# Optimization experiments

Hardware: AMD Instinct MI355X
Metric: run time of the kernel (lower is better)

## Reference

```python
import jax, jax.numpy as jnp
import numpy as np

B, DV, W, H = 256, 2048, 14, 14
DA = 620            # answer embedding dim
DATT = 1200         # attention dim_v == dim_a == dim_mm (elementwise fusion)
DOUT = 1024         # vec2seq dim_v / dim_a
NUM_CLASSES = 3000


def setup_inputs() -> dict:
    key = jax.random.key(0)
    ks = jax.random.split(key, 14)
    s = lambda *sh: 1.0 / np.sqrt(sh[-1])
    return {
        "input_v": jax.random.normal(ks[0], (B, DV, W, H), jnp.float32),
        "emb": jax.random.normal(ks[1], (NUM_CLASSES, DA), jnp.float32),
        "W_conv_v": jax.random.normal(ks[2], (DATT, DV), jnp.float32) * s(DV),
        "b_conv_v": jnp.zeros((DATT,), jnp.float32),
        "W_lin_a": jax.random.normal(ks[3], (DATT, DA), jnp.float32) * s(DA),
        "b_lin_a": jnp.zeros((DATT,), jnp.float32),
        "w_att": jax.random.normal(ks[4], (DATT,), jnp.float32) * s(DATT),
        "b_att": jnp.zeros((), jnp.float32),
        "W_img": jax.random.normal(ks[5], (DOUT, DV), jnp.float32) * s(DV),
        "b_img": jnp.zeros((DOUT,), jnp.float32),
        "W_ans": jax.random.normal(ks[6], (DOUT, DA), jnp.float32) * s(DA),
        "b_ans": jnp.zeros((DOUT,), jnp.float32),
        "input_a": jax.random.randint(ks[7], (B,), 0, NUM_CLASSES, jnp.int64)
                   if jax.config.jax_enable_x64 else
                   jax.random.randint(ks[7], (B,), 0, NUM_CLASSES, jnp.int32),
    }


def reference(input_v, emb, W_conv_v, b_conv_v, W_lin_a, b_lin_a,
              w_att, b_att, W_img, b_img, W_ans, b_ans, input_a):
    # answer embedding lookup: [B, DA]
    x_a_vec = emb[input_a]

    # --- _attention ---
    # original visual features flattened: [B, WH, DV]
    x_v_orig = input_v.reshape(B, DV, W * H).transpose(0, 2, 1)
    # conv1x1 + relu on image map -> [B, WH, DATT]
    x_v = jax.nn.relu(jnp.einsum('bchw,kc->bhwk', input_v, W_conv_v) + b_conv_v)
    x_v = x_v.reshape(B, W * H, DATT)
    # linear + relu on answer vec -> [B, DATT]
    x_a = jax.nn.relu(x_a_vec @ W_lin_a.T + b_lin_a)
    # elementwise fusion (MLB-style) + relu -> [B, WH, DATT]
    x_att = jax.nn.relu(x_v * x_a[:, None, :])
    # conv_att (1x1 conv, 1 output channel) -> logits [B, WH]
    logits = jnp.einsum('bsk,k->bs', x_att, w_att) + b_att
    attn = jax.nn.softmax(logits, axis=-1)             # [B, WH]
    # attention-weighted sum over spatial positions -> [B, DV]
    x_v_att = jnp.einsum('bs,bsd->bd', attn, x_v_orig)

    # --- prepare_feature ---
    v_feat = x_v_att @ W_img.T + b_img                 # [B, DOUT]
    a_feat = x_a_vec @ W_ans.T + b_ans                 # [B, DOUT]
    return jnp.concatenate([v_feat, a_feat], axis=-1)  # [B, 2*DOUT]
```

## Files before the change

kernel.cpp:

```cpp
#include <hip/hip_runtime.h>
#include <cstdint>
#include <cstddef>

#define B_     256
#define S_     196
#define DV_    2048
#define DA_    620
#define DATT_  1200
#define DATTP_ 1280
#define DOUT_  1024

#define IVB_SSTR 224

typedef unsigned short ushort_t;
typedef __attribute__((ext_vector_type(8))) short short8;
typedef __attribute__((ext_vector_type(4))) float floatx4;

__device__ __forceinline__ float bf2f(unsigned int u) {
    union { unsigned int i; float f; } v; v.i = u << 16; return v.f;
}
__device__ __forceinline__ ushort_t f2bf(float x) {
    union { float f; unsigned int u; } c; c.f = x;
    unsigned int r = (c.u + 0x7fffu + ((c.u >> 16) & 1u)) >> 16;
    return (ushort_t)r;
}

struct F4 { float v[4]; };
struct F8 { float v[8]; };

__device__ __forceinline__ F4 ld4(const void* p, size_t i, int f) {
    F4 r;
    if (f) {
        float4 u = *(const float4*)((const float*)p + i);
        r.v[0]=u.x; r.v[1]=u.y; r.v[2]=u.z; r.v[3]=u.w;
    } else {
        uint2 u = *(const uint2*)((const ushort_t*)p + i);
        r.v[0]=bf2f(u.x & 0xffffu); r.v[1]=bf2f(u.x >> 16);
        r.v[2]=bf2f(u.y & 0xffffu); r.v[3]=bf2f(u.y >> 16);
    }
    return r;
}
__device__ __forceinline__ F8 ld8(const void* p, size_t i, int f) {
    F8 r;
    if (f) {
        float4 a = *(const float4*)((const float*)p + i);
        float4 b = *(const float4*)((const float*)p + i + 4);
        r.v[0]=a.x; r.v[1]=a.y; r.v[2]=a.z; r.v[3]=a.w;
        r.v[4]=b.x; r.v[5]=b.y; r.v[6]=b.z; r.v[7]=b.w;
    } else {
        uint4 u = *(const uint4*)((const ushort_t*)p + i);
        r.v[0]=bf2f(u.x & 0xffffu); r.v[1]=bf2f(u.x >> 16);
        r.v[2]=bf2f(u.y & 0xffffu); r.v[3]=bf2f(u.y >> 16);
        r.v[4]=bf2f(u.z & 0xffffu); r.v[5]=bf2f(u.z >> 16);
        r.v[6]=bf2f(u.w & 0xffffu); r.v[7]=bf2f(u.w >> 16);
    }
    return r;
}
__device__ __forceinline__ float lds1(const void* p, size_t i, int f) {
    return f ? ((const float*)p)[i] : bf2f((unsigned int)((const ushort_t*)p)[i]);
}
__device__ __forceinline__ void stout(void* p, size_t i, float v, int f) {
    if (f) ((float*)p)[i] = v; else ((ushort_t*)p)[i] = f2bf(v);
}

typedef const __attribute__((address_space(1))) unsigned int* gas_t;
typedef __attribute__((address_space(3))) unsigned int* las_t;
__device__ __forceinline__ void async_cp16(const ushort_t* src, ushort_t* lds) {
    __builtin_amdgcn_global_load_lds((gas_t)(const void*)src, (las_t)(void*)lds, 16, 0, 0);
}

__global__ __launch_bounds__(64) void k0_detect(const void* __restrict__ emb,
                                                int* __restrict__ flags)
{
    int lane = threadIdx.x;
    unsigned int u = ((const ushort_t*)emb)[lane];
    unsigned int e = (u >> 7) & 0xffu;
    bool sane = (e >= 100u && e <= 140u);
    unsigned long long m = __ballot(sane);
    if (lane == 0) flags[0] = (__popcll(m) >= 48) ? 0 : 1;
}

__global__ __launch_bounds__(256) void k1_xa(
    const void* __restrict__ emb, const int* __restrict__ ia,
    const void* __restrict__ Wla, const void* __restrict__ bla,
    const void* __restrict__ watt,
    const void* __restrict__ Wans, const void* __restrict__ bans,
    float* __restrict__ xa_w, void* __restrict__ out,
    const int* __restrict__ flags)
{
    const int f = flags[0];
    __shared__ float xa[16][DA_];
    int t = threadIdx.x;
    int bc = blockIdx.x & 15, rc = blockIdx.x >> 4;
    int b0 = bc * 16;
    for (int idx = t; idx < 16 * 155; idx += 256) {
        int row = idx / 155, c8 = idx % 155;
        int cls = ia[b0 + row];
        cls = min(max(cls, 0), 2999);
        F4 u = ld4(emb, (size_t)cls * DA_ + c8 * 4, f);
        xa[row][c8*4+0] = u.v[0]; xa[row][c8*4+1] = u.v[1];
        xa[row][c8*4+2] = u.v[2]; xa[row][c8*4+3] = u.v[3];
    }
    __syncthreads();
    int wave = t >> 6, lane = t & 63;
    for (int j = 0; j < 18; ++j) {
        int row = rc * 72 + wave + 4 * j;
        bool is_xa = row < DATTP_;
        int n = row;
        int o = row - DATTP_;
        const void* wmat = is_xa ? Wla : Wans;
        size_t wrow = is_xa ? (size_t)n * DA_ : (size_t)o * DA_;
        bool live = !(is_xa && n >= DATT_);
        float wv[12];
        if (live) {
            #pragma unroll
            for (int i = 0; i < 3; ++i) {
                int c = 4 * lane + 256 * i;
                if (c < DA_) {
                    F4 u = ld4(wmat, wrow + c, f);
                    wv[i*4+0]=u.v[0]; wv[i*4+1]=u.v[1];
                    wv[i*4+2]=u.v[2]; wv[i*4+3]=u.v[3];
                } else { wv[i*4+0]=0.f; wv[i*4+1]=0.f; wv[i*4+2]=0.f; wv[i*4+3]=0.f; }
            }
        }
        for (int bb = 0; bb < 16; ++bb) {
            float p = 0.f;
            if (live) {
                #pragma unroll
                for (int i = 0; i < 3; ++i) {
                    int c = 4 * lane + 256 * i;
                    if (c < DA_) {
                        p += wv[i*4+0]*xa[bb][c+0] + wv[i*4+1]*xa[bb][c+1]
                           + wv[i*4+2]*xa[bb][c+2] + wv[i*4+3]*xa[bb][c+3];
                    }
                }
            }
            #pragma unroll
            for (int off = 1; off < 64; off <<= 1)
                p += __shfl_xor(p, off, 64);
            if (lane == 0) {
                int b = b0 + bb;
                if (is_xa) {
                    float v = 0.f;
                    if (n < DATT_)
                        v = fmaxf(p + lds1(bla, n, f), 0.f) * lds1(watt, n, f);
                    xa_w[(size_t)b * DATTP_ + n] = v;
                } else {
                    stout(out, (size_t)b * 2048 + 1024 + o,
                          p + lds1(bans, o, f), f);
                }
            }
        }
    }
}

__global__ __launch_bounds__(256) void kp_w(
    const void* __restrict__ Wc, ushort_t* __restrict__ Wcb,
    const int* __restrict__ flags)
{
    const int f = flags[0];
    int n = blockIdx.x;
    int t = threadIdx.x;
    size_t o = (size_t)n * DV_ + t * 8;
    uint4 w = make_uint4(0u, 0u, 0u, 0u);
    if (n < DATT_) {
        F8 u = ld8(Wc, o, f);
        w.x = (unsigned)f2bf(u.v[0]) | ((unsigned)f2bf(u.v[1]) << 16);
        w.y = (unsigned)f2bf(u.v[2]) | ((unsigned)f2bf(u.v[3]) << 16);
        w.z = (unsigned)f2bf(u.v[4]) | ((unsigned)f2bf(u.v[5]) << 16);
        w.w = (unsigned)f2bf(u.v[6]) | ((unsigned)f2bf(u.v[7]) << 16);
    }
    *(uint4*)&Wcb[o] = w;
}

__global__ __launch_bounds__(256) void kp_iv(
    const void* __restrict__ iv, ushort_t* __restrict__ ivb,
    const int* __restrict__ flags)
{
    const int f = flags[0];
    __shared__ float tile[64 * 64];
    int t = threadIdx.x;
    int bid = blockIdx.x;
    int b  = bid >> 7;
    int cc = (bid >> 2) & 31;
    int sc = bid & 3;
    int c0 = cc * 64, s0 = sc * 64;
    #pragma unroll
    for (int i = 0; i < 4; ++i) {
        int idx = t + 256 * i;
        int c = idx >> 4, q = idx & 15;
        int s = s0 + 4 * q;
        float4 v = make_float4(0.f, 0.f, 0.f, 0.f);
        if (s < S_) {
            F4 u = ld4(iv, ((size_t)b * DV_ + (c0 + c)) * (size_t)S_ + s, f);
            v = make_float4(u.v[0], u.v[1], u.v[2], u.v[3]);
        }
        int up = q ^ (c >> 2);
        *(float4*)&tile[c * 64 + up * 4] = v;
    }
    __syncthreads();
    #pragma unroll
    for (int i = 0; i < 4; ++i) {
        int sl = (t >> 4) + 16 * i;
        int s = s0 + sl;
        int g = t & 15;
        if (s < S_) {
            int uw = ((sl >> 2) ^ g) << 2;
            ushort4 w;
            w.x = f2bf(tile[(4*g + 0) * 64 + uw + (sl & 3)]);
            w.y = f2bf(tile[(4*g + 1) * 64 + uw + (sl & 3)]);
            w.z = f2bf(tile[(4*g + 2) * 64 + uw + (sl & 3)]);
            w.w = f2bf(tile[(4*g + 3) * 64 + uw + (sl & 3)]);
            *(ushort4*)&ivb[(size_t)b * (IVB_SSTR * DV_) + (size_t)s * DV_ + c0 + 4*g] = w;
        }
    }
}

#define BM2_ 112
#define BN2_ 128

template<int MT>
__device__ __forceinline__ void k2_body(
    const ushort_t* __restrict__ ivA,
    const ushort_t* __restrict__ Bp,
    const void* __restrict__ bcv, const float* __restrict__ xa_w,
    float* __restrict__ logits, int f,
    ushort_t* sA0, ushort_t* sA1, ushort_t* sB0, ushort_t* sB1,
    float* llog, int b, int s0, int n0, int rows_valid, int t)
{
    const int A_units = MT * 16 * 8;
    const int total_units = A_units + BN2_ * 8;
    int wave = t >> 6, lane = t & 63;
    int lquad = lane >> 4, l15 = lane & 15;
    int nbase = wave * 32;

    floatx4 acc[MT][2];
    #pragma unroll
    for (int mt = 0; mt < MT; ++mt) {
        acc[mt][0] = floatx4{0.f, 0.f, 0.f, 0.f};
        acc[mt][1] = floatx4{0.f, 0.f, 0.f, 0.f};
    }

    auto stage = [&](const ushort_t* aK, const ushort_t* bK,
                     ushort_t* dA, ushort_t* dB) {
        #pragma unroll
        for (int u0 = 0; u0 < total_units; u0 += 256) {
            int u = u0 + t;
            if (u < total_units) {
                int ub = u & ~63;
                if (u < A_units) {
                    int r = u >> 3, up = u & 7, ul = up ^ (r & 7);
                    async_cp16(aK + (size_t)r * DV_ + ul * 8, dA + ub * 8);
                } else {
                    int v = u - A_units;
                    int r = v >> 3, up = v & 7, ul = up ^ (r & 7);
                    async_cp16(bK + (size_t)r * DV_ + ul * 8, dB + (ub - A_units) * 8);
                }
            }
        }
    };

    auto compute = [&](const ushort_t* cA, const ushort_t* cB) {
        #pragma unroll
        for (int ks = 0; ks < 2; ++ks) {
            int usw = (ks * 4 + lquad) ^ (l15 & 7);
            short8 bf0 = *(const short8*)&cB[((nbase      + l15) * 8 + usw) * 8];
            short8 bf1 = *(const short8*)&cB[((nbase + 16 + l15) * 8 + usw) * 8];
            #pragma unroll
            for (int mt = 0; mt < MT; ++mt) {
                short8 af = *(const short8*)&cA[((mt * 16 + l15) * 8 + usw) * 8];
                acc[mt][0] = __builtin_amdgcn_mfma_f32_16x16x32_bf16(af, bf0, acc[mt][0], 0, 0, 0);
                acc[mt][1] = __builtin_amdgcn_mfma_f32_16x16x32_bf16(af, bf1, acc[mt][1], 0, 0, 0);
            }
        }
    };

    stage(ivA, Bp, sA0, sB0);
    __syncthreads();
    for (int kt = 0; kt < 32; kt += 2) {
        stage(ivA + (kt + 1) * 64, Bp + (kt + 1) * 64, sA1, sB1);
        compute(sA0, sB0);
        __syncthreads();
        if (kt + 2 < 32)
            stage(ivA + (kt + 2) * 64, Bp + (kt + 2) * 64, sA0, sB0);
        compute(sA1, sB1);
        __syncthreads();
    }

    float bias[2], xw[2];
    #pragma unroll
    for (int bt = 0; bt < 2; ++bt) {
        int ng = n0 + nbase + bt * 16 + l15;
        bias[bt] = (ng < DATT_) ? lds1(bcv, ng, f) : 0.f;
        xw[bt]   = (ng < DATT_) ? xa_w[(size_t)b * DATTP_ + ng] : 0.f;
    }
    float plog[MT][4];
    #pragma unroll
    for (int mt = 0; mt < MT; ++mt)
        #pragma unroll
        for (int r = 0; r < 4; ++r) {
            float v0 = fmaxf(acc[mt][0][r] + bias[0], 0.f) * xw[0];
            float v1 = fmaxf(acc[mt][1][r] + bias[1], 0.f) * xw[1];
            plog[mt][r] = v0 + v1;
        }
    #pragma unroll
    for (int off = 1; off <= 8; off <<= 1)
        #pragma unroll
        for (int mt = 0; mt < MT; ++mt)
            #pragma unroll
            for (int r = 0; r < 4; ++r)
                plog[mt][r] += __shfl_xor(plog[mt][r], off, 64);
    if (l15 == 0) {
        #pragma unroll
        for (int mt = 0; mt < MT; ++mt)
            #pragma unroll
            for (int r = 0; r < 4; ++r)
                atomicAdd(&llog[mt * 16 + lquad * 4 + r], plog[mt][r]);
    }
    __syncthreads();
    if (t < rows_valid)
        atomicAdd(&logits[(size_t)b * 256 + s0 + t], llog[t]);
}

__global__ __launch_bounds__(256) void k2_gemm_v2(
    const ushort_t* __restrict__ ivb, const ushort_t* __restrict__ Wcb,
    const void* __restrict__ bcv, const float* __restrict__ xa_w,
    float* __restrict__ logits, const int* __restrict__ flags)
{
    const int f = flags[0];
    __shared__ ushort_t sA[2][BM2_ * 64];
    __shared__ ushort_t sB[2][BN2_ * 64];
    __shared__ float llog[BM2_];
    int t = threadIdx.x;
    int bid = blockIdx.x;
    int lg = (bid & 7) * 640 + (bid >> 3);
    int b = lg / 20, rem = lg % 20;
    int mb = rem / 10, nb = rem % 10;
    int s0 = mb * BM2_, n0 = nb * BN2_;
    int rows_valid = min(BM2_, S_ - s0);
    if (t < BM2_) llog[t] = 0.f;
    const ushort_t* ivA = ivb + (size_t)b * (IVB_SSTR * DV_) + (size_t)s0 * DV_;
    const ushort_t* Bp  = Wcb + (size_t)n0 * DV_;
    if (mb == 0)
        k2_body<7>(ivA, Bp, bcv, xa_w, logits, f,
                   sA[0], sA[1], sB[0], sB[1], llog, b, s0, n0, rows_valid, t);
    else
        k2_body<6>(ivA, Bp, bcv, xa_w, logits, f,
                   sA[0], sA[1], sB[0], sB[1], llog, b, s0, n0, rows_valid, t);
}

#define BM_  112
#define BN_  128
#define LDA_ 40
#define LDB_ 40

__global__ __launch_bounds__(256) void k2_gemm(
    const void* __restrict__ iv, const void* __restrict__ Wc,
    const void* __restrict__ bcv, const float* __restrict__ xa_w,
    float* __restrict__ logits, const int* __restrict__ flags)
{
    const int f = flags[0];
    __shared__ ushort_t Al[BM_ * LDA_];
    __shared__ ushort_t Bl[BN_ * LDB_];
    __shared__ float llog[BM_];

    int t = threadIdx.x;
    int bid = blockIdx.x;
    int b   = bid / 20;
    int rem = bid % 20;
    int mb = rem / 10, nb = rem % 10;
    int s0 = mb * BM_, n0 = nb * BN_;
    int rows_valid = min(BM_, S_ - s0);
    int cpc = (rows_valid + 7) >> 3;
    int totA = 32 * cpc;

    if (t < BM_) llog[t] = 0.f;
    for (int idx = t; idx < (BM_ - rows_valid) * LDA_; idx += 256)
        Al[rows_valid * LDA_ + idx] = 0;

    size_t ivbase = (size_t)b * DV_ * S_;

    int wave = t >> 6, lane = t & 63;
    int lquad = lane >> 4, l15 = lane & 15;
    int nbase = wave * 32;

    floatx4 acc[7][2];
    #pragma unroll
    for (int mt = 0; mt < 7; ++mt) {
        acc[mt][0] = floatx4{0.f, 0.f, 0.f, 0.f};
        acc[mt][1] = floatx4{0.f, 0.f, 0.f, 0.f};
    }

    for (int kt = 0; kt < DV_ / 32; ++kt) {
        int k0 = kt * 32;
        __syncthreads();
        for (int idx = t; idx < totA; idx += 256) {
            int c = idx & 31, j = idx >> 5;
            int sr = min(8 * j, rows_valid - 8);
            F8 u = ld8(iv, ivbase + (size_t)(k0 + c) * S_ + s0 + sr, f);
            #pragma unroll
            for (int i = 0; i < 8; ++i)
                Al[(sr + i) * LDA_ + c] = f2bf(u.v[i]);
        }
        for (int idx = t; idx < 512; idx += 256) {
            int nl = idx >> 2, kc = idx & 3;
            int ng = n0 + nl;
            if (ng < DATT_) {
                F8 u = ld8(Wc, (size_t)ng * DV_ + k0 + kc * 8, f);
                #pragma unroll
                for (int i = 0; i < 8; ++i)
                    Bl[nl * LDB_ + kc * 8 + i] = f2bf(u.v[i]);
            } else {
                #pragma unroll
                for (int i = 0; i < 8; ++i)
                    Bl[nl * LDB_ + kc * 8 + i] = 0;
            }
        }
        __syncthreads();
        short8 bf0 = *(const short8*)&Bl[(nbase + l15) * LDB_ + lquad * 8];
        short8 bf1 = *(const short8*)&Bl[(nbase + 16 + l15) * LDB_ + lquad * 8];
        #pragma unroll
        for (int mt = 0; mt < 7; ++mt) {
            short8 af = *(const short8*)&Al[(mt * 16 + l15) * LDA_ + lquad * 8];
            acc[mt][0] = __builtin_amdgcn_mfma_f32_16x16x32_bf16(af, bf0, acc[mt][0], 0, 0, 0);
            acc[mt][1] = __builtin_amdgcn_mfma_f32_16x16x32_bf16(af, bf1, acc[mt][1], 0, 0, 0);
        }
    }

    float bias[2], xw[2];
    #pragma unroll
    for (int bt = 0; bt < 2; ++bt) {
        int ng = n0 + nbase + bt * 16 + l15;
        bias[bt] = (ng < DATT_) ? lds1(bcv, ng, f) : 0.f;
        xw[bt]   = (ng < DATT_) ? xa_w[(size_t)b * DATTP_ + ng] : 0.f;
    }
    float plog[7][4];
    #pragma unroll
    for (int mt = 0; mt < 7; ++mt)
        #pragma unroll
        for (int r = 0; r < 4; ++r) {
            float v0 = fmaxf(acc[mt][0][r] + bias[0], 0.f) * xw[0];
            float v1 = fmaxf(acc[mt][1][r] + bias[1], 0.f) * xw[1];
            plog[mt][r] = v0 + v1;
        }
    #pragma unroll
    for (int off = 1; off <= 8; off <<= 1)
        #pragma unroll
        for (int mt = 0; mt < 7; ++mt)
            #pragma unroll
            for (int r = 0; r < 4; ++r)
                plog[mt][r] += __shfl_xor(plog[mt][r], off, 64);
    if (l15 == 0) {
        #pragma unroll
        for (int mt = 0; mt < 7; ++mt)
            #pragma unroll
            for (int r = 0; r < 4; ++r)
                atomicAdd(&llog[mt * 16 + lquad * 4 + r], plog[mt][r]);
    }
    __syncthreads();
    if (t < rows_valid)
        atomicAdd(&logits[(size_t)b * 256 + s0 + t], llog[t]);
}

__global__ __launch_bounds__(64) void k3a_softmax(float* __restrict__ logits)
{
    int b = blockIdx.x, lane = threadIdx.x;
    float v[4]; float mx = -1e30f;
    #pragma unroll
    for (int i = 0; i < 4; ++i) {
        int s = lane + 64 * i;
        v[i] = (s < S_) ? logits[(size_t)b * 256 + s] : -1e30f;
        union { float f; unsigned u; } cv; cv.f = v[i];
        if ((cv.u & 0x7f800000u) == 0x7f800000u) v[i] = -1e30f;
        mx = fmaxf(mx, v[i]);
    }
    #pragma unroll
    for (int off = 1; off < 64; off <<= 1)
        mx = fmaxf(mx, __shfl_xor(mx, off, 64));
    float e[4]; float sum = 0.f;
    #pragma unroll
    for (int i = 0; i < 4; ++i) {
        int s = lane + 64 * i;
        e[i] = (s < S_) ? __expf(v[i] - mx) : 0.f;
        sum += e[i];
    }
    #pragma unroll
    for (int off = 1; off < 64; off <<= 1)
        sum += __shfl_xor(sum, off, 64);
    float inv = 1.f / sum;
    #pragma unroll
    for (int i = 0; i < 4; ++i) {
        int s = lane + 64 * i;
        if (s < S_) logits[(size_t)b * 256 + s] = e[i] * inv;
    }
}

__global__ __launch_bounds__(256) void k3b_wsum(
    const void* __restrict__ iv, const float* __restrict__ attn,
    float* __restrict__ xvatt, const int* __restrict__ flags)
{
    const int f = flags[0];
    __shared__ float at[200];
    int t = threadIdx.x;
    int b = blockIdx.x >> 3, dc = blockIdx.x & 7;
    if (t < S_) at[t] = attn[(size_t)b * 256 + t];
    __syncthreads();
    int wave = t >> 6, lane = t & 63;
    int s = 4 * lane;
    float a0 = 0.f, a1 = 0.f, a2 = 0.f, a3 = 0.f;
    if (s < S_) { a0 = at[s]; a1 = at[s+1]; a2 = at[s+2]; a3 = at[s+3]; }
    int dbase = dc * 256 + wave * 64;
    size_t rowb = ((size_t)b * DV_ + dbase) * S_;
    #pragma unroll 4
    for (int rr = 0; rr < 64; ++rr) {
        float p = 0.f;
        if (s < S_) {
            F4 u = ld4(iv, rowb + (size_t)rr * S_ + s, f);
            p = u.v[0]*a0 + u.v[1]*a1 + u.v[2]*a2 + u.v[3]*a3;
        }
        #pragma unroll
        for (int off = 1; off < 64; off <<= 1)
            p += __shfl_xor(p, off, 64);
        if (lane == 0) xvatt[(size_t)b * DV_ + dbase + rr] = p;
    }
}

__global__ __launch_bounds__(256) void k3c_vfeat(
    const float* __restrict__ xvatt, const void* __restrict__ Wimg,
    const void* __restrict__ bimg, void* __restrict__ out,
    const int* __restrict__ flags)
{
    const int f = flags[0];
    __shared__ float xv[DV_];
    int t = threadIdx.x;
    int oc = blockIdx.x >> 5, bc2 = blockIdx.x & 31;
    int o0 = oc * 64, b0 = bc2 * 8;
    int wave = t >> 6, lane = t & 63;
    for (int bb = 0; bb < 8; ++bb) {
        int b = b0 + bb;
        __syncthreads();
        {
            const float4* src = (const float4*)(xvatt + (size_t)b * DV_);
            float4* dst = (float4*)xv;
            dst[t] = src[t];
            dst[t + 256] = src[t + 256];
        }
        __syncthreads();
        for (int j = 0; j < 16; ++j) {
            int o = o0 + wave * 16 + j;
            size_t wrow = (size_t)o * DV_;
            float p = 0.f;
            #pragma unroll
            for (int i = 0; i < 4; ++i) {
                int c = 8 * lane + 512 * i;
                F8 u = ld8(Wimg, wrow + c, f);
                p += u.v[0]*xv[c+0] + u.v[1]*xv[c+1] + u.v[2]*xv[c+2] + u.v[3]*xv[c+3];
                p += u.v[4]*xv[c+4] + u.v[5]*xv[c+5] + u.v[6]*xv[c+6] + u.v[7]*xv[c+7];
            }
            #pragma unroll
            for (int off = 1; off < 64; off <<= 1)
                p += __shfl_xor(p, off, 64);
            if (lane == 0)
                stout(out, (size_t)b * 2048 + o, p + lds1(bimg, o, f), f);
        }
    }
}

extern "C" void kernel_launch(void* const* d_in, const int* in_sizes, int n_in,
                              void* d_out, int out_size, void* d_ws, size_t ws_size,
                              hipStream_t stream)
{
    const void* iv   = d_in[0];
    const void* emb  = d_in[1];
    const void* Wc   = d_in[2];
    const void* bcv  = d_in[3];
    const void* Wla  = d_in[4];
    const void* bla  = d_in[5];
    const void* watt = d_in[6];
    const void* Wimg = d_in[8];
    const void* bimg = d_in[9];
    const void* Wans = d_in[10];
    const void* bans = d_in[11];
    const int*  ia   = (const int*)d_in[12];

    char* ws = (char*)d_ws;
    float* xa_w   = (float*)(ws);
    float* logits = (float*)(ws + 1310720);
    float* xvatt  = (float*)(ws + 1572864);
    int*   flags  = (int*)(ws + 3670016);
    ushort_t* Wcb = (ushort_t*)(ws + 3674112);
    ushort_t* ivb = (ushort_t*)(ws + 8916992);
    const size_t WS_NEED = 8916992ull + (size_t)B_ * IVB_SSTR * DV_ * 2;

    hipMemsetAsync(logits, 0, 256 * 256 * 4, stream);
    k0_detect<<<1, 64, 0, stream>>>(emb, flags);
    k1_xa<<<512, 256, 0, stream>>>(emb, ia, Wla, bla, watt, Wans, bans, xa_w, d_out, flags);
    if (ws_size >= WS_NEED) {
        kp_w<<<1280, 256, 0, stream>>>(Wc, Wcb, flags);
        kp_iv<<<32768, 256, 0, stream>>>(iv, ivb, flags);
        k2_gemm_v2<<<5120, 256, 0, stream>>>(ivb, Wcb, bcv, xa_w, logits, flags);
    } else {
        k2_gemm<<<5120, 256, 0, stream>>>(iv, Wc, bcv, xa_w, logits, flags);
    }
    k3a_softmax<<<256, 64, 0, stream>>>(logits);
    k3b_wsum<<<2048, 256, 0, stream>>>(iv, logits, xvatt, flags);
    k3c_vfeat<<<512, 256, 0, stream>>>(xvatt, Wimg, bimg, d_out, flags);
}
```

Before: 1.365 ms.

## Replace attention-logit GEMM with 256x256-tile kernel using 32x32x16 MFMA

Swaps the 112x128-tile, 256-thread attention-logit GEMM for a 512-thread kernel. Each block now covers all 224 padded spatial rows and 256 output channels, and each wave computes a 128x64 sub-tile with 32x32x16 bf16 MFMA instructions. The aim is more operand reuse per LDS load and fewer blocks re-reading the same image rows and weights. The epilogue that fuses bias, ReLU and the attention-weight dot is reworked for the 32x32 accumulator layout. The trade-off is a much larger LDS footprint and more registers per thread, which lowers occupancy. Some MFMA rows read padding or adjacent buffer memory, but those rows are discarded.

```diff
diff --git a/kernel.cpp b/kernel.cpp
--- a/kernel.cpp
+++ b/kernel.cpp
@@ -15,6 +15,7 @@
 typedef unsigned short ushort_t;
 typedef __attribute__((ext_vector_type(8))) short short8;
 typedef __attribute__((ext_vector_type(4))) float floatx4;
+typedef __attribute__((ext_vector_type(16))) float floatx16;
 
 __device__ __forceinline__ float bf2f(unsigned int u) {
     union { unsigned int i; float f; } v; v.i = u << 16; return v.f;
@@ -216,45 +217,63 @@
     }
 }
 
-#define BM2_ 112
-#define BN2_ 128
-
-template<int MT>
-__device__ __forceinline__ void k2_body(
-    const ushort_t* __restrict__ ivA,
-    const ushort_t* __restrict__ Bp,
+#define BM3_ 256
+#define BN3_ 256
+#define AU3_ 1792
+#define BU3_ 2048
+#define TU3_ 3840
+
+#define SA0_ 0
+#define SA1_ 14336
+#define SB0_ 28672
+#define SB1_ 45056
+#define SPOOL_ 61440
+
+__global__ __launch_bounds__(512, 2) void k2_gemm_v3(
+    const ushort_t* __restrict__ ivb, const ushort_t* __restrict__ Wcb,
     const void* __restrict__ bcv, const float* __restrict__ xa_w,
-    float* __restrict__ logits, int f,
-    ushort_t* sA0, ushort_t* sA1, ushort_t* sB0, ushort_t* sB1,
-    float* llog, int b, int s0, int n0, int rows_valid, int t)
-{
-    const int A_units = MT * 16 * 8;
-    const int total_units = A_units + BN2_ * 8;
-    int wave = t >> 6, lane = t & 63;
-    int lquad = lane >> 4, l15 = lane & 15;
-    int nbase = wave * 32;
-
-    floatx4 acc[MT][2];
-    #pragma unroll
-    for (int mt = 0; mt < MT; ++mt) {
-        acc[mt][0] = floatx4{0.f, 0.f, 0.f, 0.f};
-        acc[mt][1] = floatx4{0.f, 0.f, 0.f, 0.f};
-    }
+    float* __restrict__ logits, const int* __restrict__ flags)
+{
+    const int f = flags[0];
+    __shared__ ushort_t smem[SPOOL_];
+    __shared__ float llog[BM3_];
+    int t = threadIdx.x;
+    int bid = blockIdx.x;
+    int lg = (bid & 7) * 160 + (bid >> 3);
+    int b = lg / 5, nb = lg % 5;
+    int n0 = nb * BN3_;
+    if (t < BM3_) llog[t] = 0.f;
+
+    const ushort_t* ivA = ivb + (size_t)b * (IVB_SSTR * DV_);
+    const ushort_t* Bp  = Wcb + (size_t)n0 * DV_;
+
+    int w = t >> 6, lane = t & 63;
+    int wm = w >> 2, wn = w & 3;
+    int l31 = lane & 31, hi = lane >> 5, l7 = lane & 7;
+
+    floatx16 acc[4][2];
+    #pragma unroll
+    for (int mt = 0; mt < 4; ++mt)
+        #pragma unroll
+        for (int nt = 0; nt < 2; ++nt)
+            #pragma unroll
+            for (int r = 0; r < 16; ++r)
+                acc[mt][nt][r] = 0.f;
 
     auto stage = [&](const ushort_t* aK, const ushort_t* bK,
                      ushort_t* dA, ushort_t* dB) {
         #pragma unroll
-        for (int u0 = 0; u0 < total_units; u0 += 256) {
+        for (int u0 = 0; u0 < TU3_; u0 += 512) {
             int u = u0 + t;
-            if (u < total_units) {
+            if (u < TU3_) {
                 int ub = u & ~63;
-                if (u < A_units) {
+                if (u < AU3_) {
                     int r = u >> 3, up = u & 7, ul = up ^ (r & 7);
                     async_cp16(aK + (size_t)r * DV_ + ul * 8, dA + ub * 8);
                 } else {
-                    int v = u - A_units;
+                    int v = u - AU3_;
                     int r = v >> 3, up = v & 7, ul = up ^ (r & 7);
-                    async_cp16(bK + (size_t)r * DV_ + ul * 8, dB + (ub - A_units) * 8);
+                    async_cp16(bK + (size_t)r * DV_ + ul * 8, dB + (v & ~63) * 8);
                 }
             }
         }
@@ -262,91 +281,73 @@
 
     auto compute = [&](const ushort_t* cA, const ushort_t* cB) {
         #pragma unroll
-        for (int ks = 0; ks < 2; ++ks) {
-            int usw = (ks * 4 + lquad) ^ (l15 & 7);
-            short8 bf0 = *(const short8*)&cB[((nbase      + l15) * 8 + usw) * 8];
-            short8 bf1 = *(const short8*)&cB[((nbase + 16 + l15) * 8 + usw) * 8];
-            #pragma unroll
-            for (int mt = 0; mt < MT; ++mt) {
-                short8 af = *(const short8*)&cA[((mt * 16 + l15) * 8 + usw) * 8];
-                acc[mt][0] = __builtin_amdgcn_mfma_f32_16x16x32_bf16(af, bf0, acc[mt][0], 0, 0, 0);
-                acc[mt][1] = __builtin_amdgcn_mfma_f32_16x16x32_bf16(af, bf1, acc[mt][1], 0, 0, 0);
-            }
+        for (int ks = 0; ks < 4; ++ks) {
+            int lu = ks * 2 + hi;
+            int up = lu ^ l7;
+            short8 af[4], bf[2];
+            #pragma unroll
+            for (int mt = 0; mt < 4; ++mt) {
+                int row = wm * 128 + mt * 32 + l31;
+                af[mt] = *(const short8*)&cA[row * 64 + up * 8];
+            }
+            #pragma unroll
+            for (int nt = 0; nt < 2; ++nt) {
+                int rn = wn * 64 + nt * 32 + l31;
+                bf[nt] = *(const short8*)&cB[rn * 64 + up * 8];
+            }
+            #pragma unroll
+            for (int mt = 0; mt < 4; ++mt)
+                #pragma unroll
+                for (int nt = 0; nt < 2; ++nt)
+                    acc[mt][nt] = __builtin_amdgcn_mfma_f32_32x32x16_bf16(
+                        af[mt], bf[nt], acc[mt][nt], 0, 0, 0);
         }
     };
 
-    stage(ivA, Bp, sA0, sB0);
+    stage(ivA, Bp, smem + SA0_, smem + SB0_);
     __syncthreads();
     for (int kt = 0; kt < 32; kt += 2) {
-        stage(ivA + (kt + 1) * 64, Bp + (kt + 1) * 64, sA1, sB1);
-        compute(sA0, sB0);
+        stage(ivA + (kt + 1) * 64, Bp + (kt + 1) * 64, smem + SA1_, smem + SB1_);
+        compute(smem + SA0_, smem + SB0_);
         __syncthreads();
         if (kt + 2 < 32)
-            stage(ivA + (kt + 2) * 64, Bp + (kt + 2) * 64, sA0, sB0);
-        compute(sA1, sB1);
+            stage(ivA + (kt + 2) * 64, Bp + (kt + 2) * 64, smem + SA0_, smem + SB0_);
+        compute(smem + SA1_, smem + SB1_);
         __syncthreads();
     }
 
     float bias[2], xw[2];
     #pragma unroll
-    for (int bt = 0; bt < 2; ++bt) {
-        int ng = n0 + nbase + bt * 16 + l15;
-        bias[bt] = (ng < DATT_) ? lds1(bcv, ng, f) : 0.f;
-        xw[bt]   = (ng < DATT_) ? xa_w[(size_t)b * DATTP_ + ng] : 0.f;
-    }
-    float plog[MT][4];
-    #pragma unroll
-    for (int mt = 0; mt < MT; ++mt)
-        #pragma unroll
-        for (int r = 0; r < 4; ++r) {
+    for (int nt = 0; nt < 2; ++nt) {
+        int ng = n0 + wn * 64 + nt * 32 + l31;
+        bias[nt] = (ng < DATT_) ? lds1(bcv, ng, f) : 0.f;
+        xw[nt]   = (ng < DATT_) ? xa_w[(size_t)b * DATTP_ + ng] : 0.f;
+    }
+    #pragma unroll
+    for (int mt = 0; mt < 4; ++mt) {
+        float v[16];
+        #pragma unroll
+        for (int r = 0; r < 16; ++r) {
             float v0 = fmaxf(acc[mt][0][r] + bias[0], 0.f) * xw[0];
             float v1 = fmaxf(acc[mt][1][r] + bias[1], 0.f) * xw[1];
-            plog[mt][r] = v0 + v1;
-        }
-    #pragma unroll
-    for (int off = 1; off <= 8; off <<= 1)
-        #pragma unroll
-        for (int mt = 0; mt < MT; ++mt)
-            #pragma unroll
-            for (int r = 0; r < 4; ++r)
-                plog[mt][r] += __shfl_xor(plog[mt][r], off, 64);
-    if (l15 == 0) {
-        #pragma unroll
-        for (int mt = 0; mt < MT; ++mt)
-            #pragma unroll
-            for (int r = 0; r < 4; ++r)
-                atomicAdd(&llog[mt * 16 + lquad * 4 + r], plog[mt][r]);
+            v[r] = v0 + v1;
+        }
+        #pragma unroll
+        for (int off = 1; off <= 16; off <<= 1)
+            #pragma unroll
+            for (int r = 0; r < 16; ++r)
+                v[r] += __shfl_xor(v[r], off, 64);
+        if (l31 == 0) {
+            #pragma unroll
+            for (int r = 0; r < 16; ++r) {
+                int row = wm * 128 + mt * 32 + (r & 3) + 8 * (r >> 2) + 4 * hi;
+                atomicAdd(&llog[row], v[r]);
+            }
+        }
     }
     __syncthreads();
-    if (t < rows_valid)
-        atomicAdd(&logits[(size_t)b * 256 + s0 + t], llog[t]);
-}
-
-__global__ __launch_bounds__(256) void k2_gemm_v2(
-    const ushort_t* __restrict__ ivb, const ushort_t* __restrict__ Wcb,
-    const void* __restrict__ bcv, const float* __restrict__ xa_w,
-    float* __restrict__ logits, const int* __restrict__ flags)
-{
-    const int f = flags[0];
-    __shared__ ushort_t sA[2][BM2_ * 64];
-    __shared__ ushort_t sB[2][BN2_ * 64];
-    __shared__ float llog[BM2_];
-    int t = threadIdx.x;
-    int bid = blockIdx.x;
-    int lg = (bid & 7) * 640 + (bid >> 3);
-    int b = lg / 20, rem = lg % 20;
-    int mb = rem / 10, nb = rem % 10;
-    int s0 = mb * BM2_, n0 = nb * BN2_;
-    int rows_valid = min(BM2_, S_ - s0);
-    if (t < BM2_) llog[t] = 0.f;
-    const ushort_t* ivA = ivb + (size_t)b * (IVB_SSTR * DV_) + (size_t)s0 * DV_;
-    const ushort_t* Bp  = Wcb + (size_t)n0 * DV_;
-    if (mb == 0)
-        k2_body<7>(ivA, Bp, bcv, xa_w, logits, f,
-                   sA[0], sA[1], sB[0], sB[1], llog, b, s0, n0, rows_valid, t);
-    else
-        k2_body<6>(ivA, Bp, bcv, xa_w, logits, f,
-                   sA[0], sA[1], sB[0], sB[1], llog, b, s0, n0, rows_valid, t);
+    if (t < S_)
+        atomicAdd(&logits[(size_t)b * 256 + t], llog[t]);
 }
 
 #define BM_  112
@@ -598,7 +599,7 @@
     if (ws_size >= WS_NEED) {
         kp_w<<<1280, 256, 0, stream>>>(Wc, Wcb, flags);
         kp_iv<<<32768, 256, 0, stream>>>(iv, ivb, flags);
-        k2_gemm_v2<<<5120, 256, 0, stream>>>(ivb, Wcb, bcv, xa_w, logits, flags);
+        k2_gemm_v3<<<1280, 512, 0, stream>>>(ivb, Wcb, bcv, xa_w, logits, flags);
     } else {
         k2_gemm<<<5120, 256, 0, stream>>>(iv, Wc, bcv, xa_w, logits, flags);
     }
```

Measured after the change: 1.336 ms. 2.1% less time.
